# Optimization experiments

Measured on AMD Instinct MI355X. Metric: run time of the kernel, lower is better.

The kernel has to match this reference:

```python
import jax, jax.numpy as jnp
import numpy as np

B, E, H, W = 32, 512, 16, 16
NH, HD = 8, 64          # num_heads = embed_dim // num_heads_channels, head_dim = 64
OUT = 512
S = H * W + 1           # spacial_dim**2 + 1 = 257 (mean token prepended)


def setup_inputs() -> dict:
    key = jax.random.key(0)
    ks = jax.random.split(key, 10)
    sc = 1.0 / np.sqrt(E).astype(np.float32)
    n = lambda k, sh, s=1.0: jax.random.normal(k, sh, jnp.float32) * s
    return {
        "x_real": n(ks[0], (B, E, H, W)),
        "x_imag": n(ks[1], (B, E, H, W)),
        # positional_embedding = (randn/sqrt(E)).to(complex64) -> imag part is zero
        "pos_r": n(ks[2], (E, S), sc),
        "pos_i": jnp.zeros((E, S), jnp.float32),
        # complex in-projection (packed q,k,v) and out-projection of the MHA
        "w_in_r": n(ks[3], (3 * E, E), sc),
        "w_in_i": n(ks[4], (3 * E, E), sc),
        "b_in_r": jnp.zeros((3 * E,), jnp.float32),
        "b_in_i": jnp.zeros((3 * E,), jnp.float32),
        "w_out_r": n(ks[5], (E, E), sc),
        "w_out_i": n(ks[6], (E, E), sc),
        "b_out_r": jnp.zeros((E,), jnp.float32),
        "b_out_i": jnp.zeros((E,), jnp.float32),
        # complex 1x1 conv projection == complex linear over channels
        "w_p_r": n(ks[7], (OUT, E), sc),
        "w_p_i": n(ks[8], (OUT, E), sc),
        "b_p_r": jnp.zeros((OUT,), jnp.float32),
        "b_p_i": jnp.zeros((OUT,), jnp.float32),
    }


def _attention_pool(x_real, x_imag, pos_r, pos_i, w_in_r, w_in_i, b_in_r, b_in_i,
                    w_out_r, w_out_i, b_out_r, b_out_i, w_p_r, w_p_i, b_p_r, b_p_i):
    cx = jax.lax.complex
    x = cx(x_real, x_imag).reshape(B, E, -1)                       # [b,c,HW]
    x = jnp.concatenate([x.mean(-1, keepdims=True), x], axis=-1)   # [b,c,S]
    x = x + cx(pos_r, pos_i)[None]                                 # + pos embed
    x = x.transpose(0, 2, 1)                                       # [b,S,E]

    qkv = jnp.einsum('bse,fe->bsf', x, cx(w_in_r, w_in_i)) + cx(b_in_r, b_in_i)
    q, k, v = jnp.split(qkv, 3, axis=-1)
    q = q.reshape(B, S, NH, HD) / jnp.sqrt(jnp.float32(HD))
    k = k.reshape(B, S, NH, HD)
    v = v.reshape(B, S, NH, HD)

    logits = jnp.einsum('bqhd,bkhd->bhqk', q, k)                   # complex scores
    # complex softmax handled separately on real/imag parts
    w = cx(jax.nn.softmax(logits.real, axis=-1),
           jax.nn.softmax(logits.imag, axis=-1))
    attn = jnp.einsum('bhqk,bkhd->bqhd', w, v).reshape(B, S, E)
    attn = jnp.einsum('bse,fe->bsf', attn, cx(w_out_r, w_out_i)) + cx(b_out_r, b_out_i)

    y = attn.transpose(0, 2, 1)                                    # [b,E,S]
    y = jnp.einsum('oc,bcs->bos', cx(w_p_r, w_p_i), y) + cx(b_p_r, b_p_i)[None, :, None]
    return y[:, :, 0]                                              # [b,OUT] complex64


def reference(x_real, x_imag, pos_r, pos_i, w_in_r, w_in_i, b_in_r, b_in_i,
              w_out_r, w_out_i, b_out_r, b_out_i, w_p_r, w_p_i, b_p_r, b_p_i):
    return _attention_pool(x_real, x_imag, pos_r, pos_i, w_in_r, w_in_i, b_in_r,
                           b_in_i, w_out_r, w_out_i, b_out_r, b_out_i,
                           w_p_r, w_p_i, b_p_r, b_p_i)
```

## Files before the change

kernel.cpp:

```cpp
#include <hip/hip_runtime.h>

#define B_   32
#define E_   512
#define HW_  256
#define S_   257
#define NH_  8
#define HD_  64
#define ECH_ 16
#define NCH_ 32
#define NBLK 1024
#define NTHR 256
#define NGRP 32
#define GSZ  32

__device__ __forceinline__ void st_sys(float* p, float v) {
  __hip_atomic_store(p, v, __ATOMIC_RELAXED, __HIP_MEMORY_SCOPE_SYSTEM);
}
__device__ __forceinline__ void st_sys2(float2* p, float2 v) {
  unsigned long long u;
  __builtin_memcpy(&u, &v, 8);
  __hip_atomic_store((unsigned long long*)p, u, __ATOMIC_RELAXED, __HIP_MEMORY_SCOPE_SYSTEM);
}

__device__ __forceinline__ float wave_reduce(float v) {
  #pragma unroll
  for (int o = 32; o > 0; o >>= 1) v += __shfl_down(v, o, 64);
  return v;
}

__device__ __forceinline__ void gbar(unsigned* slots, int g, int j, int t, unsigned phase) {
  __syncthreads();
  if (t < 64) {
    if (t == 0)
      __hip_atomic_store(&slots[g * GSZ + j], phase, __ATOMIC_RELAXED, __HIP_MEMORY_SCOPE_SYSTEM);
    const unsigned* line = slots + g * GSZ;
    int sl = t & 31;
    for (;;) {
      unsigned v = __hip_atomic_load(&line[sl], __ATOMIC_RELAXED, __HIP_MEMORY_SCOPE_SYSTEM);
      if (__all((int)(v >= phase))) break;
      __builtin_amdgcn_s_sleep(2);
    }
  }
  __syncthreads();
}

__device__ void softmax257(float* l, float* red, int t) {
  float v = l[t];
  float v256 = l[256];
  red[t] = v; __syncthreads();
  #pragma unroll
  for (int s = 128; s > 0; s >>= 1) { if (t < s) red[t] = fmaxf(red[t], red[t + s]); __syncthreads(); }
  float M = fmaxf(red[0], v256);
  __syncthreads();
  float ex = expf(v - M);
  float e256 = expf(v256 - M);
  red[t] = ex; __syncthreads();
  #pragma unroll
  for (int s = 128; s > 0; s >>= 1) { if (t < s) red[t] += red[t + s]; __syncthreads(); }
  float inv = 1.f / (red[0] + e256);
  __syncthreads();
  l[t] = ex * inv;
  if (t == 0) l[256] = e256 * inv;
  __syncthreads();
}

__global__ __launch_bounds__(NTHR, 4) void k_mega(
    const float* __restrict__ xr, const float* __restrict__ xi,
    const float* __restrict__ pos_r, const float* __restrict__ pos_i,
    const float* __restrict__ w_in_r, const float* __restrict__ w_in_i,
    const float* __restrict__ b_in_r, const float* __restrict__ b_in_i,
    const float* __restrict__ w_out_r, const float* __restrict__ w_out_i,
    const float* __restrict__ b_out_r, const float* __restrict__ b_out_i,
    const float* __restrict__ w_p_r, const float* __restrict__ w_p_i,
    const float* __restrict__ b_p_r, const float* __restrict__ b_p_i,
    unsigned* slots,
    float* __restrict__ mr, float* __restrict__ mi,
    float* __restrict__ q0r, float* __restrict__ q0i,
    float* __restrict__ l0pr, float* __restrict__ l0pi,
    float* __restrict__ part, float* __restrict__ w2,
    float* __restrict__ zr_, float* __restrict__ zi_,
    float* __restrict__ a0r, float* __restrict__ a0i,
    float* __restrict__ aor, float* __restrict__ aoi,
    float* __restrict__ out, int interleaved) {
  __shared__ __align__(16) float smF[4112];
  const int t   = threadIdx.x;
  const int l   = t & 63;
  const int w   = t >> 6;
  const int bid = blockIdx.x;
  const int g   = bid >> 5;
  const int j   = bid & 31;

  #pragma unroll
  for (int rr = 0; rr < 4; ++rr) {
    int e = j * 16 + w * 4 + rr;
    float4 vr = ((const float4*)(xr + ((size_t)g * E_ + e) * HW_))[l];
    float4 vi = ((const float4*)(xi + ((size_t)g * E_ + e) * HW_))[l];
    float sr = (vr.x + vr.y) + (vr.z + vr.w);
    float si = (vi.x + vi.y) + (vi.z + vi.w);
    sr = wave_reduce(sr); si = wave_reduce(si);
    if (l == 0) {
      st_sys(&mr[g * E_ + e], sr * (1.f / HW_) + pos_r[(size_t)e * S_]);
      st_sys(&mi[g * E_ + e], si * (1.f / HW_) + pos_i[(size_t)e * S_]);
    }
  }
  gbar(slots, g, j, t, 1);

  {
    float* mR = smF;
    float* mI = smF + 512;
    mR[t]       = mr[g * E_ + t];        mI[t]       = mi[g * E_ + t];
    mR[t + 256] = mr[g * E_ + t + 256];  mI[t + 256] = mi[g * E_ + t + 256];
    __syncthreads();
    #pragma unroll
    for (int rr = 0; rr < 4; ++rr) {
      int f = j * 16 + w * 4 + rr;
      const float* wr = w_in_r + (size_t)f * E_;
      const float* wi = w_in_i + (size_t)f * E_;
      float ar = 0.f, ai = 0.f;
      #pragma unroll
      for (int e = l; e < E_; e += 64) {
        float Xr = mR[e], Xi = mI[e], Cr = wr[e], Ci = wi[e];
        ar += Xr * Cr - Xi * Ci;
        ai += Xr * Ci + Xi * Cr;
      }
      ar = wave_reduce(ar); ai = wave_reduce(ai);
      if (l == 0) {
        st_sys(&q0r[g * E_ + f], (ar + b_in_r[f]) * 0.125f);
        st_sys(&q0i[g * E_ + f], (ai + b_in_i[f]) * 0.125f);
      }
    }
  }
  gbar(slots, g, j, t, 2);

  {
    int c = j, e0 = c * ECH_;
    float* q0s = smF;
    float* us  = smF + 1024;
    float* mS  = smF + 1280;
    { int f0 = t * 2;
      q0s[f0 * 2 + 0]       = q0r[g * E_ + f0];
      q0s[f0 * 2 + 1]       = q0i[g * E_ + f0];
      q0s[(f0 + 1) * 2 + 0] = q0r[g * E_ + f0 + 1];
      q0s[(f0 + 1) * 2 + 1] = q0i[g * E_ + f0 + 1];
      if (t < ECH_) { mS[t * 2] = mr[g * E_ + e0 + t]; mS[t * 2 + 1] = mi[g * E_ + e0 + t]; }
    }
    __syncthreads();
    if (t < 128) {
      int e = t & 15, hh = t >> 4;
      float ar = 0.f, ai = 0.f;
      #pragma unroll 8
      for (int d = 0; d < HD_; ++d) {
        int f = hh * HD_ + d;
        float qr = q0s[f * 2], qi = q0s[f * 2 + 1];
        float Wr = w_in_r[(size_t)(E_ + f) * E_ + e0 + e];
        float Wi = w_in_i[(size_t)(E_ + f) * E_ + e0 + e];
        ar += qr * Wr - qi * Wi;
        ai += qr * Wi + qi * Wr;
      }
      us[(e * 8 + hh) * 2 + 0] = ar;
      us[(e * 8 + hh) * 2 + 1] = ai;
    }
    __syncthreads();
    if (t < NH_) {
      float pr = 0.f, pi = 0.f;
      #pragma unroll
      for (int e = 0; e < ECH_; ++e) {
        float Xr = mS[e * 2], Xi = mS[e * 2 + 1];
        float Ur = us[(e * 8 + t) * 2], Ui = us[(e * 8 + t) * 2 + 1];
        pr += Xr * Ur - Xi * Ui;
        pi += Xr * Ui + Xi * Ur;
      }
      st_sys(&l0pr[((size_t)g * NH_ + t) * NCH_ + c], pr);
      st_sys(&l0pi[((size_t)g * NH_ + t) * NCH_ + c], pi);
    }
    float ar[NH_], ai[NH_];
    #pragma unroll
    for (int hh = 0; hh < NH_; ++hh) { ar[hh] = 0.f; ai[hh] = 0.f; }
    const float* xrb = xr + ((size_t)g * E_ + e0) * HW_;
    const float* xib = xi + ((size_t)g * E_ + e0) * HW_;
    #pragma unroll 2
    for (int e = 0; e < ECH_; ++e) {
      float Xr = xrb[e * HW_ + t] + pos_r[(size_t)(e0 + e) * S_ + t + 1];
      float Xi = xib[e * HW_ + t] + pos_i[(size_t)(e0 + e) * S_ + t + 1];
      #pragma unroll
      for (int hh = 0; hh < NH_; ++hh) {
        float Ur = us[(e * 8 + hh) * 2], Ui = us[(e * 8 + hh) * 2 + 1];
        ar[hh] += Xr * Ur - Xi * Ui;
        ai[hh] += Xr * Ui + Xi * Ur;
      }
    }
    float2* p2 = (float2*)part;
    #pragma unroll
    for (int hh = 0; hh < NH_; ++hh) {
      float2 v; v.x = ar[hh]; v.y = ai[hh];
      st_sys2(&p2[(((size_t)g * NH_ + hh) * NCH_ + c) * 256 + t], v);
    }
  }
  gbar(slots, g, j, t, 3);

  if (j < NH_) {
    int bh = g * NH_ + j;
    float* lr  = smF;
    float* li  = smF + 260;
    float* red = smF + 520;
    const float2* p2 = (const float2*)part + (size_t)bh * NCH_ * 256;
    float sr = 0.f, si = 0.f;
    #pragma unroll
    for (int c = 0; c < NCH_; ++c) { float2 v = p2[c * 256 + t]; sr += v.x; si += v.y; }
    lr[t + 1] = sr; li[t + 1] = si;
    if (t < 64) {
      float v = (t < NCH_) ? l0pr[(size_t)bh * NCH_ + t] : 0.f;
      v = wave_reduce(v);
      if (t == 0) lr[0] = v;
    } else if (t < 128) {
      int tt = t - 64;
      float v = (tt < NCH_) ? l0pi[(size_t)bh * NCH_ + tt] : 0.f;
      v = wave_reduce(v);
      if (tt == 0) li[0] = v;
    }
    __syncthreads();
    softmax257(lr, red, t);
    softmax257(li, red, t);
    float2* o = (float2*)w2 + (size_t)bh * S_;
    float2 v; v.x = lr[t]; v.y = li[t];
    st_sys2(&o[t], v);
    if (t == 0) { float2 v2; v2.x = lr[256]; v2.y = li[256]; st_sys2(&o[256], v2); }
  }
  gbar(slots, g, j, t, 4);

  {
    float2* wls = (float2*)smF;
    const float2* w2b = (const float2*)w2 + (size_t)g * NH_ * S_;
    for (int i = t; i < NH_ * S_; i += NTHR) wls[i] = w2b[i];
    __syncthreads();
    #pragma unroll
    for (int sub = 0; sub < 2; ++sub) {
      int gq = j + sub * 32;
      #pragma unroll
      for (int r = 0; r < 2; ++r) {
        int e = gq * 8 + w * 2 + r;
        const float* xre = xr + ((size_t)g * E_ + e) * HW_;
        const float* xie = xi + ((size_t)g * E_ + e) * HW_;
        const float* pre = pos_r + (size_t)e * S_;
        const float* pie = pos_i + (size_t)e * S_;
        float ar2[NH_], ai2[NH_];
        #pragma unroll
        for (int hh = 0; hh < NH_; ++hh) { ar2[hh] = 0.f; ai2[hh] = 0.f; }
        #pragma unroll
        for (int jj = 0; jj < 4; ++jj) {
          int k = 1 + l + 64 * jj;
          float Xr = xre[k - 1] + pre[k];
          float Xi = xie[k - 1] + pie[k];
          #pragma unroll
          for (int hh = 0; hh < NH_; ++hh) {
            float2 W = wls[hh * S_ + k];
            ar2[hh] += W.x * Xr - W.y * Xi;
            ai2[hh] += W.x * Xi + W.y * Xr;
          }
        }
        #pragma unroll
        for (int hh = 0; hh < NH_; ++hh) { ar2[hh] = wave_reduce(ar2[hh]); ai2[hh] = wave_reduce(ai2[hh]); }
        if (l == 0) {
          float X0r = mr[g * E_ + e];
          float X0i = mi[g * E_ + e];
          #pragma unroll
          for (int hh = 0; hh < NH_; ++hh) {
            float2 W0 = wls[hh * S_];
            st_sys(&zr_[(size_t)(g * NH_ + hh) * E_ + e], ar2[hh] + W0.x * X0r - W0.y * X0i);
            st_sys(&zi_[(size_t)(g * NH_ + hh) * E_ + e], ai2[hh] + W0.x * X0i + W0.y * X0r);
          }
        }
      }
    }
  }
  gbar(slots, g, j, t, 5);

  #pragma unroll
  for (int rr = 0; rr < 4; ++rr) {
    int f = j * 16 + w * 4 + rr;
    int h = f >> 6;
    const float* wrp = w_in_r + (size_t)(2 * E_ + f) * E_;
    const float* wip = w_in_i + (size_t)(2 * E_ + f) * E_;
    const float* zrp = zr_ + (size_t)(g * NH_ + h) * E_;
    const float* zip = zi_ + (size_t)(g * NH_ + h) * E_;
    float ar = 0.f, ai = 0.f;
    #pragma unroll
    for (int e = l; e < E_; e += 64) {
      float Zr = zrp[e], Zi = zip[e], Cr = wrp[e], Ci = wip[e];
      ar += Zr * Cr - Zi * Ci;
      ai += Zr * Ci + Zi * Cr;
    }
    ar = wave_reduce(ar); ai = wave_reduce(ai);
    if (l == 0) {
      float bvr = b_in_r[2 * E_ + f], bvi = b_in_i[2 * E_ + f];
      st_sys(&a0r[g * E_ + f], ar + (bvr - bvi));
      st_sys(&a0i[g * E_ + f], ai + (bvr + bvi));
    }
  }
  gbar(slots, g, j, t, 6);

  #pragma unroll
  for (int rr = 0; rr < 4; ++rr) {
    int f = j * 16 + w * 4 + rr;
    const float* wrp = w_out_r + (size_t)f * E_;
    const float* wip = w_out_i + (size_t)f * E_;
    const float* ir = a0r + (size_t)g * E_;
    const float* ii = a0i + (size_t)g * E_;
    float ar = 0.f, ai = 0.f;
    #pragma unroll
    for (int e = l; e < E_; e += 64) {
      float Xr = ir[e], Xi = ii[e], Cr = wrp[e], Ci = wip[e];
      ar += Xr * Cr - Xi * Ci;
      ai += Xr * Ci + Xi * Cr;
    }
    ar = wave_reduce(ar); ai = wave_reduce(ai);
    if (l == 0) { st_sys(&aor[g * E_ + f], ar + b_out_r[f]); st_sys(&aoi[g * E_ + f], ai + b_out_i[f]); }
  }
  gbar(slots, g, j, t, 7);

  #pragma unroll
  for (int rr = 0; rr < 4; ++rr) {
    int f = j * 16 + w * 4 + rr;
    const float* wrp = w_p_r + (size_t)f * E_;
    const float* wip = w_p_i + (size_t)f * E_;
    const float* ir = aor + (size_t)g * E_;
    const float* ii = aoi + (size_t)g * E_;
    float ar = 0.f, ai = 0.f;
    #pragma unroll
    for (int e = l; e < E_; e += 64) {
      float Xr = ir[e], Xi = ii[e], Cr = wrp[e], Ci = wip[e];
      ar += Xr * Cr - Xi * Ci;
      ai += Xr * Ci + Xi * Cr;
    }
    ar = wave_reduce(ar); ai = wave_reduce(ai);
    if (l == 0) {
      float rr2 = ar + b_p_r[f];
      float im  = ai + b_p_i[f];
      int wid = g * E_ + f;
      if (interleaved) { out[(size_t)wid * 2] = rr2; out[(size_t)wid * 2 + 1] = im; }
      else             { out[wid] = rr2; }
    }
  }
}

extern "C" void kernel_launch(void* const* d_in, const int* in_sizes, int n_in,
                              void* d_out, int out_size, void* d_ws, size_t ws_size,
                              hipStream_t stream) {
  (void)in_sizes; (void)n_in; (void)ws_size;
  const float* xr      = (const float*)d_in[0];
  const float* xi      = (const float*)d_in[1];
  const float* pos_r   = (const float*)d_in[2];
  const float* pos_i   = (const float*)d_in[3];
  const float* w_in_r  = (const float*)d_in[4];
  const float* w_in_i  = (const float*)d_in[5];
  const float* b_in_r  = (const float*)d_in[6];
  const float* b_in_i  = (const float*)d_in[7];
  const float* w_out_r = (const float*)d_in[8];
  const float* w_out_i = (const float*)d_in[9];
  const float* b_out_r = (const float*)d_in[10];
  const float* b_out_i = (const float*)d_in[11];
  const float* w_p_r   = (const float*)d_in[12];
  const float* w_p_i   = (const float*)d_in[13];
  const float* b_p_r   = (const float*)d_in[14];
  const float* b_p_i   = (const float*)d_in[15];

  const int BE = B_ * E_, BHE = B_ * NH_ * E_;
  unsigned* slots = (unsigned*)d_ws;
  float* base = (float*)d_ws + 1024;
  float* mr   = base;
  float* mi   = mr   + BE;
  float* q0r  = mi   + BE;
  float* q0i  = q0r  + BE;
  float* l0pr = q0i  + BE;
  float* l0pi = l0pr + B_ * NH_ * NCH_;
  float* part = l0pi + B_ * NH_ * NCH_;
  float* w2   = part + (size_t)B_ * NH_ * NCH_ * 512;
  float* zr   = w2   + (size_t)2 * B_ * NH_ * S_;
  float* zi   = zr   + BHE;
  float* a0r  = zi   + BHE;
  float* a0i  = a0r  + BE;
  float* aor  = a0i  + BE;
  float* aoi  = aor  + BE;

  hipMemsetAsync(d_ws, 0, 4096, stream);
  k_mega<<<NBLK, NTHR, 0, stream>>>(
      xr, xi, pos_r, pos_i, w_in_r, w_in_i, b_in_r, b_in_i,
      w_out_r, w_out_i, b_out_r, b_out_i, w_p_r, w_p_i, b_p_r, b_p_i,
      slots, mr, mi, q0r, q0i, l0pr, l0pi, part, w2, zr, zi, a0r, a0i, aor, aoi,
      (float*)d_out, out_size >= 2 * B_ * E_);
}
```

Baseline: 202.3 us.

## Prefetch next-phase weights before barriers and use shuffle softmax reductions

```diff
diff --git a/kernel.cpp b/kernel.cpp
--- a/kernel.cpp
+++ b/kernel.cpp
@@ -45,20 +45,23 @@
 }
 
 __device__ void softmax257(float* l, float* red, int t) {
+  int lane = t & 63, wv = t >> 6;
   float v = l[t];
   float v256 = l[256];
-  red[t] = v; __syncthreads();
-  #pragma unroll
-  for (int s = 128; s > 0; s >>= 1) { if (t < s) red[t] = fmaxf(red[t], red[t + s]); __syncthreads(); }
-  float M = fmaxf(red[0], v256);
+  float m = v;
+  #pragma unroll
+  for (int o = 32; o > 0; o >>= 1) m = fmaxf(m, __shfl_xor(m, o, 64));
+  if (lane == 0) red[wv] = m;
   __syncthreads();
+  float M = fmaxf(fmaxf(fmaxf(red[0], red[1]), fmaxf(red[2], red[3])), v256);
   float ex = expf(v - M);
   float e256 = expf(v256 - M);
-  red[t] = ex; __syncthreads();
-  #pragma unroll
-  for (int s = 128; s > 0; s >>= 1) { if (t < s) red[t] += red[t + s]; __syncthreads(); }
-  float inv = 1.f / (red[0] + e256);
+  float s = ex;
+  #pragma unroll
+  for (int o = 32; o > 0; o >>= 1) s += __shfl_xor(s, o, 64);
+  if (lane == 0) red[4 + wv] = s;
   __syncthreads();
+  float inv = 1.f / (red[4] + red[5] + red[6] + red[7] + e256);
   l[t] = ex * inv;
   if (t == 0) l[256] = e256 * inv;
   __syncthreads();
@@ -89,6 +92,7 @@
   const int bid = blockIdx.x;
   const int g   = bid >> 5;
   const int j   = bid & 31;
+  float pfacc = 0.f;
 
   #pragma unroll
   for (int rr = 0; rr < 4; ++rr) {
@@ -103,6 +107,17 @@
       st_sys(&mi[g * E_ + e], si * (1.f / HW_) + pos_i[(size_t)e * S_]);
     }
   }
+  {
+    int row = 16 * j + (t >> 4);
+    int c32 = (t & 15) * 32;
+    pfacc += w_in_r[(size_t)row * E_ + c32] + w_in_i[(size_t)row * E_ + c32];
+    size_t colk = (size_t)16 * j;
+    pfacc += w_in_r[(size_t)(E_ + t) * E_ + colk] + w_in_i[(size_t)(E_ + t) * E_ + colk];
+    pfacc += w_in_r[(size_t)(E_ + t + 256) * E_ + colk] + w_in_i[(size_t)(E_ + t + 256) * E_ + colk];
+    int pcol = (t & 15) * 16 + 1;
+    pfacc += pos_r[(size_t)row * S_ + pcol] + pos_i[(size_t)row * S_ + pcol];
+  }
+  asm volatile("" :: "v"(pfacc));
   gbar(slots, g, j, t, 1);
 
   {
@@ -234,45 +249,45 @@
     for (int i = t; i < NH_ * S_; i += NTHR) wls[i] = w2b[i];
     __syncthreads();
     #pragma unroll
-    for (int sub = 0; sub < 2; ++sub) {
-      int gq = j + sub * 32;
-      #pragma unroll
-      for (int r = 0; r < 2; ++r) {
-        int e = gq * 8 + w * 2 + r;
-        const float* xre = xr + ((size_t)g * E_ + e) * HW_;
-        const float* xie = xi + ((size_t)g * E_ + e) * HW_;
-        const float* pre = pos_r + (size_t)e * S_;
-        const float* pie = pos_i + (size_t)e * S_;
-        float ar2[NH_], ai2[NH_];
+    for (int rr = 0; rr < 4; ++rr) {
+      int e = 16 * j + 4 * w + rr;
+      const float* xre = xr + ((size_t)g * E_ + e) * HW_;
+      const float* xie = xi + ((size_t)g * E_ + e) * HW_;
+      const float* pre = pos_r + (size_t)e * S_;
+      const float* pie = pos_i + (size_t)e * S_;
+      float ar2[NH_], ai2[NH_];
+      #pragma unroll
+      for (int hh = 0; hh < NH_; ++hh) { ar2[hh] = 0.f; ai2[hh] = 0.f; }
+      #pragma unroll
+      for (int jj = 0; jj < 4; ++jj) {
+        int k = 1 + l + 64 * jj;
+        float Xr = xre[k - 1] + pre[k];
+        float Xi = xie[k - 1] + pie[k];
         #pragma unroll
-        for (int hh = 0; hh < NH_; ++hh) { ar2[hh] = 0.f; ai2[hh] = 0.f; }
+        for (int hh = 0; hh < NH_; ++hh) {
+          float2 W = wls[hh * S_ + k];
+          ar2[hh] += W.x * Xr - W.y * Xi;
+          ai2[hh] += W.x * Xi + W.y * Xr;
+        }
+      }
+      #pragma unroll
+      for (int hh = 0; hh < NH_; ++hh) { ar2[hh] = wave_reduce(ar2[hh]); ai2[hh] = wave_reduce(ai2[hh]); }
+      if (l == 0) {
+        float X0r = mr[g * E_ + e];
+        float X0i = mi[g * E_ + e];
         #pragma unroll
-        for (int jj = 0; jj < 4; ++jj) {
-          int k = 1 + l + 64 * jj;
-          float Xr = xre[k - 1] + pre[k];
-          float Xi = xie[k - 1] + pie[k];
-          #pragma unroll
-          for (int hh = 0; hh < NH_; ++hh) {
-            float2 W = wls[hh * S_ + k];
-            ar2[hh] += W.x * Xr - W.y * Xi;
-            ai2[hh] += W.x * Xi + W.y * Xr;
-          }
+        for (int hh = 0; hh < NH_; ++hh) {
+          float2 W0 = wls[hh * S_];
+          st_sys(&zr_[(size_t)(g * NH_ + hh) * E_ + e], ar2[hh] + W0.x * X0r - W0.y * X0i);
+          st_sys(&zi_[(size_t)(g * NH_ + hh) * E_ + e], ai2[hh] + W0.x * X0i + W0.y * X0r);
         }
-        #pragma unroll
-        for (int hh = 0; hh < NH_; ++hh) { ar2[hh] = wave_reduce(ar2[hh]); ai2[hh] = wave_reduce(ai2[hh]); }
-        if (l == 0) {
-          float X0r = mr[g * E_ + e];
-          float X0i = mi[g * E_ + e];
-          #pragma unroll
-          for (int hh = 0; hh < NH_; ++hh) {
-            float2 W0 = wls[hh * S_];
-            st_sys(&zr_[(size_t)(g * NH_ + hh) * E_ + e], ar2[hh] + W0.x * X0r - W0.y * X0i);
-            st_sys(&zi_[(size_t)(g * NH_ + hh) * E_ + e], ai2[hh] + W0.x * X0i + W0.y * X0r);
-          }
-        }
-      }
-    }
-  }
+      }
+    }
+    int row = 16 * j + (t >> 4);
+    int c32 = (t & 15) * 32;
+    pfacc += w_in_r[(size_t)(2 * E_ + row) * E_ + c32] + w_in_i[(size_t)(2 * E_ + row) * E_ + c32];
+  }
+  asm volatile("" :: "v"(pfacc));
   gbar(slots, g, j, t, 5);
 
   #pragma unroll
@@ -297,6 +312,12 @@
       st_sys(&a0i[g * E_ + f], ai + (bvr + bvi));
     }
   }
+  {
+    int row = 16 * j + (t >> 4);
+    int c32 = (t & 15) * 32;
+    pfacc += w_out_r[(size_t)row * E_ + c32] + w_out_i[(size_t)row * E_ + c32];
+  }
+  asm volatile("" :: "v"(pfacc));
   gbar(slots, g, j, t, 6);
 
   #pragma unroll
@@ -316,6 +337,12 @@
     ar = wave_reduce(ar); ai = wave_reduce(ai);
     if (l == 0) { st_sys(&aor[g * E_ + f], ar + b_out_r[f]); st_sys(&aoi[g * E_ + f], ai + b_out_i[f]); }
   }
+  {
+    int row = 16 * j + (t >> 4);
+    int c32 = (t & 15) * 32;
+    pfacc += w_p_r[(size_t)row * E_ + c32] + w_p_i[(size_t)row * E_ + c32];
+  }
+  asm volatile("" :: "v"(pfacc));
   gbar(slots, g, j, t, 7);
 
   #pragma unroll
```

After: 212.9 us. 5.2% more time.

## Double block count per batch group and use wave-shuffle softmax reductions

Applied to the files above, without the earlier changes.

```diff
diff --git a/kernel.cpp b/kernel.cpp
--- a/kernel.cpp
+++ b/kernel.cpp
@@ -6,12 +6,12 @@
 #define S_   257
 #define NH_  8
 #define HD_  64
-#define ECH_ 16
-#define NCH_ 32
-#define NBLK 1024
+#define ECH_ 8
+#define NCH_ 64
+#define NBLK 2048
 #define NTHR 256
 #define NGRP 32
-#define GSZ  32
+#define GSZ  64
 
 __device__ __forceinline__ void st_sys(float* p, float v) {
   __hip_atomic_store(p, v, __ATOMIC_RELAXED, __HIP_MEMORY_SCOPE_SYSTEM);
@@ -34,9 +34,8 @@
     if (t == 0)
       __hip_atomic_store(&slots[g * GSZ + j], phase, __ATOMIC_RELAXED, __HIP_MEMORY_SCOPE_SYSTEM);
     const unsigned* line = slots + g * GSZ;
-    int sl = t & 31;
     for (;;) {
-      unsigned v = __hip_atomic_load(&line[sl], __ATOMIC_RELAXED, __HIP_MEMORY_SCOPE_SYSTEM);
+      unsigned v = __hip_atomic_load(&line[t], __ATOMIC_RELAXED, __HIP_MEMORY_SCOPE_SYSTEM);
       if (__all((int)(v >= phase))) break;
       __builtin_amdgcn_s_sleep(2);
     }
@@ -45,26 +44,29 @@
 }
 
 __device__ void softmax257(float* l, float* red, int t) {
+  int lane = t & 63, wv = t >> 6;
   float v = l[t];
   float v256 = l[256];
-  red[t] = v; __syncthreads();
-  #pragma unroll
-  for (int s = 128; s > 0; s >>= 1) { if (t < s) red[t] = fmaxf(red[t], red[t + s]); __syncthreads(); }
-  float M = fmaxf(red[0], v256);
-  __syncthreads();
+  float m = v;
+  #pragma unroll
+  for (int o = 32; o > 0; o >>= 1) m = fmaxf(m, __shfl_xor(m, o, 64));
+  if (lane == 0) red[wv] = m;
+  __syncthreads();
+  float M = fmaxf(fmaxf(fmaxf(red[0], red[1]), fmaxf(red[2], red[3])), v256);
   float ex = expf(v - M);
   float e256 = expf(v256 - M);
-  red[t] = ex; __syncthreads();
-  #pragma unroll
-  for (int s = 128; s > 0; s >>= 1) { if (t < s) red[t] += red[t + s]; __syncthreads(); }
-  float inv = 1.f / (red[0] + e256);
-  __syncthreads();
+  float s = ex;
+  #pragma unroll
+  for (int o = 32; o > 0; o >>= 1) s += __shfl_xor(s, o, 64);
+  if (lane == 0) red[4 + wv] = s;
+  __syncthreads();
+  float inv = 1.f / (red[4] + red[5] + red[6] + red[7] + e256);
   l[t] = ex * inv;
   if (t == 0) l[256] = e256 * inv;
   __syncthreads();
 }
 
-__global__ __launch_bounds__(NTHR, 4) void k_mega(
+__global__ __launch_bounds__(NTHR, 8) void k_mega(
     const float* __restrict__ xr, const float* __restrict__ xi,
     const float* __restrict__ pos_r, const float* __restrict__ pos_i,
     const float* __restrict__ w_in_r, const float* __restrict__ w_in_i,
@@ -87,12 +89,12 @@
   const int l   = t & 63;
   const int w   = t >> 6;
   const int bid = blockIdx.x;
-  const int g   = bid >> 5;
-  const int j   = bid & 31;
-
-  #pragma unroll
-  for (int rr = 0; rr < 4; ++rr) {
-    int e = j * 16 + w * 4 + rr;
+  const int g   = bid >> 6;
+  const int j   = bid & 63;
+
+  #pragma unroll
+  for (int rr = 0; rr < 2; ++rr) {
+    int e = j * 8 + w * 2 + rr;
     float4 vr = ((const float4*)(xr + ((size_t)g * E_ + e) * HW_))[l];
     float4 vi = ((const float4*)(xi + ((size_t)g * E_ + e) * HW_))[l];
     float sr = (vr.x + vr.y) + (vr.z + vr.w);
@@ -112,8 +114,8 @@
     mR[t + 256] = mr[g * E_ + t + 256];  mI[t + 256] = mi[g * E_ + t + 256];
     __syncthreads();
     #pragma unroll
-    for (int rr = 0; rr < 4; ++rr) {
-      int f = j * 16 + w * 4 + rr;
+    for (int rr = 0; rr < 2; ++rr) {
+      int f = j * 8 + w * 2 + rr;
       const float* wr = w_in_r + (size_t)f * E_;
       const float* wi = w_in_i + (size_t)f * E_;
       float ar = 0.f, ai = 0.f;
@@ -136,7 +138,8 @@
     int c = j, e0 = c * ECH_;
     float* q0s = smF;
     float* us  = smF + 1024;
-    float* mS  = smF + 1280;
+    float* pu  = smF + 1152;
+    float* mS  = smF + 1664;
     { int f0 = t * 2;
       q0s[f0 * 2 + 0]       = q0r[g * E_ + f0];
       q0s[f0 * 2 + 1]       = q0i[g * E_ + f0];
@@ -145,20 +148,27 @@
       if (t < ECH_) { mS[t * 2] = mr[g * E_ + e0 + t]; mS[t * 2 + 1] = mi[g * E_ + e0 + t]; }
     }
     __syncthreads();
-    if (t < 128) {
-      int e = t & 15, hh = t >> 4;
+    {
+      int e = t & 7, hh = (t >> 3) & 7, dq = t >> 6;
       float ar = 0.f, ai = 0.f;
-      #pragma unroll 8
-      for (int d = 0; d < HD_; ++d) {
-        int f = hh * HD_ + d;
+      #pragma unroll
+      for (int dd = 0; dd < 16; ++dd) {
+        int f = hh * HD_ + dq * 16 + dd;
         float qr = q0s[f * 2], qi = q0s[f * 2 + 1];
         float Wr = w_in_r[(size_t)(E_ + f) * E_ + e0 + e];
         float Wi = w_in_i[(size_t)(E_ + f) * E_ + e0 + e];
         ar += qr * Wr - qi * Wi;
         ai += qr * Wi + qi * Wr;
       }
-      us[(e * 8 + hh) * 2 + 0] = ar;
-      us[(e * 8 + hh) * 2 + 1] = ai;
+      pu[(dq * 64 + e * 8 + hh) * 2 + 0] = ar;
+      pu[(dq * 64 + e * 8 + hh) * 2 + 1] = ai;
+    }
+    __syncthreads();
+    if (t < 128) {
+      int e = t & 7, hh = (t >> 3) & 7, ri = t >> 6;
+      us[(e * 8 + hh) * 2 + ri] =
+          pu[(0 * 64 + e * 8 + hh) * 2 + ri] + pu[(1 * 64 + e * 8 + hh) * 2 + ri] +
+          pu[(2 * 64 + e * 8 + hh) * 2 + ri] + pu[(3 * 64 + e * 8 + hh) * 2 + ri];
     }
     __syncthreads();
     if (t < NH_) {
@@ -205,16 +215,16 @@
     float* red = smF + 520;
     const float2* p2 = (const float2*)part + (size_t)bh * NCH_ * 256;
     float sr = 0.f, si = 0.f;
-    #pragma unroll
+    #pragma unroll 8
     for (int c = 0; c < NCH_; ++c) { float2 v = p2[c * 256 + t]; sr += v.x; si += v.y; }
     lr[t + 1] = sr; li[t + 1] = si;
     if (t < 64) {
-      float v = (t < NCH_) ? l0pr[(size_t)bh * NCH_ + t] : 0.f;
+      float v = l0pr[(size_t)bh * NCH_ + t];
       v = wave_reduce(v);
       if (t == 0) lr[0] = v;
     } else if (t < 128) {
       int tt = t - 64;
-      float v = (tt < NCH_) ? l0pi[(size_t)bh * NCH_ + tt] : 0.f;
+      float v = l0pi[(size_t)bh * NCH_ + tt];
       v = wave_reduce(v);
       if (tt == 0) li[0] = v;
     }
@@ -234,50 +244,46 @@
     for (int i = t; i < NH_ * S_; i += NTHR) wls[i] = w2b[i];
     __syncthreads();
     #pragma unroll
-    for (int sub = 0; sub < 2; ++sub) {
-      int gq = j + sub * 32;
-      #pragma unroll
-      for (int r = 0; r < 2; ++r) {
-        int e = gq * 8 + w * 2 + r;
-        const float* xre = xr + ((size_t)g * E_ + e) * HW_;
-        const float* xie = xi + ((size_t)g * E_ + e) * HW_;
-        const float* pre = pos_r + (size_t)e * S_;
-        const float* pie = pos_i + (size_t)e * S_;
-        float ar2[NH_], ai2[NH_];
+    for (int rr = 0; rr < 2; ++rr) {
+      int e = 8 * j + 2 * w + rr;
+      const float* xre = xr + ((size_t)g * E_ + e) * HW_;
+      const float* xie = xi + ((size_t)g * E_ + e) * HW_;
+      const float* pre = pos_r + (size_t)e * S_;
+      const float* pie = pos_i + (size_t)e * S_;
+      float ar2[NH_], ai2[NH_];
+      #pragma unroll
+      for (int hh = 0; hh < NH_; ++hh) { ar2[hh] = 0.f; ai2[hh] = 0.f; }
+      #pragma unroll
+      for (int jj = 0; jj < 4; ++jj) {
+        int k = 1 + l + 64 * jj;
+        float Xr = xre[k - 1] + pre[k];
+        float Xi = xie[k - 1] + pie[k];
         #pragma unroll
-        for (int hh = 0; hh < NH_; ++hh) { ar2[hh] = 0.f; ai2[hh] = 0.f; }
+        for (int hh = 0; hh < NH_; ++hh) {
+          float2 W = wls[hh * S_ + k];
+          ar2[hh] += W.x * Xr - W.y * Xi;
+          ai2[hh] += W.x * Xi + W.y * Xr;
+        }
+      }
+      #pragma unroll
+      for (int hh = 0; hh < NH_; ++hh) { ar2[hh] = wave_reduce(ar2[hh]); ai2[hh] = wave_reduce(ai2[hh]); }
+      if (l == 0) {
+        float X0r = mr[g * E_ + e];
+        float X0i = mi[g * E_ + e];
         #pragma unroll
-        for (int jj = 0; jj < 4; ++jj) {
-          int k = 1 + l + 64 * jj;
-          float Xr = xre[k - 1] + pre[k];
-          float Xi = xie[k - 1] + pie[k];
-          #pragma unroll
-          for (int hh = 0; hh < NH_; ++hh) {
-            float2 W = wls[hh * S_ + k];
-            ar2[hh] += W.x * Xr - W.y * Xi;
-            ai2[hh] += W.x * Xi + W.y * Xr;
-          }
+        for (int hh = 0; hh < NH_; ++hh) {
+          float2 W0 = wls[hh * S_];
+          st_sys(&zr_[(size_t)(g * NH_ + hh) * E_ + e], ar2[hh] + W0.x * X0r - W0.y * X0i);
+          st_sys(&zi_[(size_t)(g * NH_ + hh) * E_ + e], ai2[hh] + W0.x * X0i + W0.y * X0r);
         }
-        #pragma unroll
-        for (int hh = 0; hh < NH_; ++hh) { ar2[hh] = wave_reduce(ar2[hh]); ai2[hh] = wave_reduce(ai2[hh]); }
-        if (l == 0) {
-          float X0r = mr[g * E_ + e];
-          float X0i = mi[g * E_ + e];
-          #pragma unroll
-          for (int hh = 0; hh < NH_; ++hh) {
-            float2 W0 = wls[hh * S_];
-            st_sys(&zr_[(size_t)(g * NH_ + hh) * E_ + e], ar2[hh] + W0.x * X0r - W0.y * X0i);
-            st_sys(&zi_[(size_t)(g * NH_ + hh) * E_ + e], ai2[hh] + W0.x * X0i + W0.y * X0r);
-          }
-        }
       }
     }
   }
   gbar(slots, g, j, t, 5);
 
   #pragma unroll
-  for (int rr = 0; rr < 4; ++rr) {
-    int f = j * 16 + w * 4 + rr;
+  for (int rr = 0; rr < 2; ++rr) {
+    int f = j * 8 + w * 2 + rr;
     int h = f >> 6;
     const float* wrp = w_in_r + (size_t)(2 * E_ + f) * E_;
     const float* wip = w_in_i + (size_t)(2 * E_ + f) * E_;
@@ -300,8 +306,8 @@
   gbar(slots, g, j, t, 6);
 
   #pragma unroll
-  for (int rr = 0; rr < 4; ++rr) {
-    int f = j * 16 + w * 4 + rr;
+  for (int rr = 0; rr < 2; ++rr) {
+    int f = j * 8 + w * 2 + rr;
     const float* wrp = w_out_r + (size_t)f * E_;
     const float* wip = w_out_i + (size_t)f * E_;
     const float* ir = a0r + (size_t)g * E_;
@@ -319,8 +325,8 @@
   gbar(slots, g, j, t, 7);
 
   #pragma unroll
-  for (int rr = 0; rr < 4; ++rr) {
-    int f = j * 16 + w * 4 + rr;
+  for (int rr = 0; rr < 2; ++rr) {
+    int f = j * 8 + w * 2 + rr;
     const float* wrp = w_p_r + (size_t)f * E_;
     const float* wip = w_p_i + (size_t)f * E_;
     const float* ir = aor + (size_t)g * E_;
@@ -366,7 +372,7 @@
 
   const int BE = B_ * E_, BHE = B_ * NH_ * E_;
   unsigned* slots = (unsigned*)d_ws;
-  float* base = (float*)d_ws + 1024;
+  float* base = (float*)d_ws + 4096;
   float* mr   = base;
   float* mi   = mr   + BE;
   float* q0r  = mi   + BE;
@@ -382,7 +388,7 @@
   float* aor  = a0i  + BE;
   float* aoi  = aor  + BE;
 
-  hipMemsetAsync(d_ws, 0, 4096, stream);
+  hipMemsetAsync(d_ws, 0, 16384, stream);
   k_mega<<<NBLK, NTHR, 0, stream>>>(
       xr, xi, pos_r, pos_i, w_in_r, w_in_i, b_in_r, b_in_i,
       w_out_r, w_out_i, b_out_r, b_out_i, w_p_r, w_p_i, b_p_r, b_p_i,
```

Result: slower. 284.4 us (+40.6%).

## Fuse q0 and key-weight product via atomics, drop partial-logit buffers, shuffle softmax

Applied to the files above, without the earlier changes.

```diff
diff --git a/kernel.cpp b/kernel.cpp
--- a/kernel.cpp
+++ b/kernel.cpp
@@ -5,13 +5,11 @@
 #define HW_  256
 #define S_   257
 #define NH_  8
-#define HD_  64
-#define ECH_ 16
-#define NCH_ 32
 #define NBLK 1024
 #define NTHR 256
 #define NGRP 32
 #define GSZ  32
+#define LG_  260
 
 __device__ __forceinline__ void st_sys(float* p, float v) {
   __hip_atomic_store(p, v, __ATOMIC_RELAXED, __HIP_MEMORY_SCOPE_SYSTEM);
@@ -45,20 +43,23 @@
 }
 
 __device__ void softmax257(float* l, float* red, int t) {
+  int lane = t & 63, wv = t >> 6;
   float v = l[t];
   float v256 = l[256];
-  red[t] = v; __syncthreads();
-  #pragma unroll
-  for (int s = 128; s > 0; s >>= 1) { if (t < s) red[t] = fmaxf(red[t], red[t + s]); __syncthreads(); }
-  float M = fmaxf(red[0], v256);
-  __syncthreads();
+  float m = v;
+  #pragma unroll
+  for (int o = 32; o > 0; o >>= 1) m = fmaxf(m, __shfl_xor(m, o, 64));
+  if (lane == 0) red[wv] = m;
+  __syncthreads();
+  float M = fmaxf(fmaxf(fmaxf(red[0], red[1]), fmaxf(red[2], red[3])), v256);
   float ex = expf(v - M);
   float e256 = expf(v256 - M);
-  red[t] = ex; __syncthreads();
-  #pragma unroll
-  for (int s = 128; s > 0; s >>= 1) { if (t < s) red[t] += red[t + s]; __syncthreads(); }
-  float inv = 1.f / (red[0] + e256);
-  __syncthreads();
+  float s = ex;
+  #pragma unroll
+  for (int o = 32; o > 0; o >>= 1) s += __shfl_xor(s, o, 64);
+  if (lane == 0) red[4 + wv] = s;
+  __syncthreads();
+  float inv = 1.f / (red[4] + red[5] + red[6] + red[7] + e256);
   l[t] = ex * inv;
   if (t == 0) l[256] = e256 * inv;
   __syncthreads();
@@ -74,10 +75,10 @@
     const float* __restrict__ w_p_r, const float* __restrict__ w_p_i,
     const float* __restrict__ b_p_r, const float* __restrict__ b_p_i,
     unsigned* slots,
+    float* __restrict__ ur_, float* __restrict__ ui_,
+    float* __restrict__ lgr, float* __restrict__ lgi,
     float* __restrict__ mr, float* __restrict__ mi,
-    float* __restrict__ q0r, float* __restrict__ q0i,
-    float* __restrict__ l0pr, float* __restrict__ l0pi,
-    float* __restrict__ part, float* __restrict__ w2,
+    float* __restrict__ w2,
     float* __restrict__ zr_, float* __restrict__ zi_,
     float* __restrict__ a0r, float* __restrict__ a0i,
     float* __restrict__ aor, float* __restrict__ aoi,
@@ -106,14 +107,16 @@
   gbar(slots, g, j, t, 1);
 
   {
-    float* mR = smF;
-    float* mI = smF + 512;
+    float* mR  = smF;
+    float* mI  = smF + 512;
+    float* q0L = smF + 1024;
     mR[t]       = mr[g * E_ + t];        mI[t]       = mi[g * E_ + t];
     mR[t + 256] = mr[g * E_ + t + 256];  mI[t + 256] = mi[g * E_ + t + 256];
     __syncthreads();
     #pragma unroll
     for (int rr = 0; rr < 4; ++rr) {
-      int f = j * 16 + w * 4 + rr;
+      int fl = w * 4 + rr;
+      int f  = 16 * j + fl;
       const float* wr = w_in_r + (size_t)f * E_;
       const float* wi = w_in_i + (size_t)f * E_;
       float ar = 0.f, ai = 0.f;
@@ -125,61 +128,45 @@
       }
       ar = wave_reduce(ar); ai = wave_reduce(ai);
       if (l == 0) {
-        st_sys(&q0r[g * E_ + f], (ar + b_in_r[f]) * 0.125f);
-        st_sys(&q0i[g * E_ + f], (ai + b_in_i[f]) * 0.125f);
-      }
-    }
+        q0L[fl * 2]     = (ar + b_in_r[f]) * 0.125f;
+        q0L[fl * 2 + 1] = (ai + b_in_i[f]) * 0.125f;
+      }
+    }
+    __syncthreads();
+    int h = j >> 2;
+    float u0r = 0.f, u0i = 0.f, u1r = 0.f, u1i = 0.f;
+    #pragma unroll 4
+    for (int fl = 0; fl < 16; ++fl) {
+      int f = 16 * j + fl;
+      float qr = q0L[fl * 2], qi = q0L[fl * 2 + 1];
+      const float* Wr = w_in_r + (size_t)(E_ + f) * E_;
+      const float* Wi = w_in_i + (size_t)(E_ + f) * E_;
+      float W0r = Wr[t], W0i = Wi[t], W1r = Wr[t + 256], W1i = Wi[t + 256];
+      u0r += qr * W0r - qi * W0i;  u0i += qr * W0i + qi * W0r;
+      u1r += qr * W1r - qi * W1i;  u1i += qr * W1i + qi * W1r;
+    }
+    size_t ub = (size_t)(g * NH_ + h) * E_;
+    atomicAdd(&ur_[ub + t], u0r);        atomicAdd(&ui_[ub + t], u0i);
+    atomicAdd(&ur_[ub + t + 256], u1r);  atomicAdd(&ui_[ub + t + 256], u1i);
   }
   gbar(slots, g, j, t, 2);
 
   {
-    int c = j, e0 = c * ECH_;
-    float* q0s = smF;
-    float* us  = smF + 1024;
-    float* mS  = smF + 1280;
-    { int f0 = t * 2;
-      q0s[f0 * 2 + 0]       = q0r[g * E_ + f0];
-      q0s[f0 * 2 + 1]       = q0i[g * E_ + f0];
-      q0s[(f0 + 1) * 2 + 0] = q0r[g * E_ + f0 + 1];
-      q0s[(f0 + 1) * 2 + 1] = q0i[g * E_ + f0 + 1];
-      if (t < ECH_) { mS[t * 2] = mr[g * E_ + e0 + t]; mS[t * 2 + 1] = mi[g * E_ + e0 + t]; }
-    }
-    __syncthreads();
+    int e0 = 16 * j;
+    float* us = smF;
     if (t < 128) {
       int e = t & 15, hh = t >> 4;
-      float ar = 0.f, ai = 0.f;
-      #pragma unroll 8
-      for (int d = 0; d < HD_; ++d) {
-        int f = hh * HD_ + d;
-        float qr = q0s[f * 2], qi = q0s[f * 2 + 1];
-        float Wr = w_in_r[(size_t)(E_ + f) * E_ + e0 + e];
-        float Wi = w_in_i[(size_t)(E_ + f) * E_ + e0 + e];
-        ar += qr * Wr - qi * Wi;
-        ai += qr * Wi + qi * Wr;
-      }
-      us[(e * 8 + hh) * 2 + 0] = ar;
-      us[(e * 8 + hh) * 2 + 1] = ai;
-    }
-    __syncthreads();
-    if (t < NH_) {
-      float pr = 0.f, pi = 0.f;
-      #pragma unroll
-      for (int e = 0; e < ECH_; ++e) {
-        float Xr = mS[e * 2], Xi = mS[e * 2 + 1];
-        float Ur = us[(e * 8 + t) * 2], Ui = us[(e * 8 + t) * 2 + 1];
-        pr += Xr * Ur - Xi * Ui;
-        pi += Xr * Ui + Xi * Ur;
-      }
-      st_sys(&l0pr[((size_t)g * NH_ + t) * NCH_ + c], pr);
-      st_sys(&l0pi[((size_t)g * NH_ + t) * NCH_ + c], pi);
-    }
+      us[(e * 8 + hh) * 2]     = ur_[(size_t)(g * NH_ + hh) * E_ + e0 + e];
+      us[(e * 8 + hh) * 2 + 1] = ui_[(size_t)(g * NH_ + hh) * E_ + e0 + e];
+    }
+    __syncthreads();
     float ar[NH_], ai[NH_];
     #pragma unroll
     for (int hh = 0; hh < NH_; ++hh) { ar[hh] = 0.f; ai[hh] = 0.f; }
     const float* xrb = xr + ((size_t)g * E_ + e0) * HW_;
     const float* xib = xi + ((size_t)g * E_ + e0) * HW_;
     #pragma unroll 2
-    for (int e = 0; e < ECH_; ++e) {
+    for (int e = 0; e < 16; ++e) {
       float Xr = xrb[e * HW_ + t] + pos_r[(size_t)(e0 + e) * S_ + t + 1];
       float Xi = xib[e * HW_ + t] + pos_i[(size_t)(e0 + e) * S_ + t + 1];
       #pragma unroll
@@ -189,11 +176,11 @@
         ai[hh] += Xr * Ui + Xi * Ur;
       }
     }
-    float2* p2 = (float2*)part;
     #pragma unroll
     for (int hh = 0; hh < NH_; ++hh) {
-      float2 v; v.x = ar[hh]; v.y = ai[hh];
-      st_sys2(&p2[(((size_t)g * NH_ + hh) * NCH_ + c) * 256 + t], v);
+      size_t lb = (size_t)(g * NH_ + hh) * LG_ + t + 1;
+      atomicAdd(&lgr[lb], ar[hh]);
+      atomicAdd(&lgi[lb], ai[hh]);
     }
   }
   gbar(slots, g, j, t, 3);
@@ -202,29 +189,38 @@
     int bh = g * NH_ + j;
     float* lr  = smF;
     float* li  = smF + 260;
-    float* red = smF + 520;
-    const float2* p2 = (const float2*)part + (size_t)bh * NCH_ * 256;
-    float sr = 0.f, si = 0.f;
-    #pragma unroll
-    for (int c = 0; c < NCH_; ++c) { float2 v = p2[c * 256 + t]; sr += v.x; si += v.y; }
-    lr[t + 1] = sr; li[t + 1] = si;
-    if (t < 64) {
-      float v = (t < NCH_) ? l0pr[(size_t)bh * NCH_ + t] : 0.f;
-      v = wave_reduce(v);
-      if (t == 0) lr[0] = v;
-    } else if (t < 128) {
-      int tt = t - 64;
-      float v = (tt < NCH_) ? l0pi[(size_t)bh * NCH_ + tt] : 0.f;
-      v = wave_reduce(v);
-      if (tt == 0) li[0] = v;
-    }
-    __syncthreads();
-    softmax257(lr, red, t);
-    softmax257(li, red, t);
+    float* redl = smF + 520;
+    float* reds = smF + 528;
+    lr[t + 1] = lgr[(size_t)bh * LG_ + t + 1];
+    li[t + 1] = lgi[(size_t)bh * LG_ + t + 1];
+    float pr = 0.f, pi = 0.f;
+    #pragma unroll
+    for (int e = t; e < E_; e += 256) {
+      float Xr = mr[g * E_ + e], Xi = mi[g * E_ + e];
+      float Ur = ur_[(size_t)bh * E_ + e], Ui = ui_[(size_t)bh * E_ + e];
+      pr += Xr * Ur - Xi * Ui;
+      pi += Xr * Ui + Xi * Ur;
+    }
+    pr = wave_reduce(pr); pi = wave_reduce(pi);
+    if (l == 0) { redl[w * 2] = pr; redl[w * 2 + 1] = pi; }
+    __syncthreads();
+    if (t == 0) {
+      lr[0] = redl[0] + redl[2] + redl[4] + redl[6];
+      li[0] = redl[1] + redl[3] + redl[5] + redl[7];
+    }
+    __syncthreads();
+    softmax257(lr, reds, t);
+    softmax257(li, reds, t);
     float2* o = (float2*)w2 + (size_t)bh * S_;
     float2 v; v.x = lr[t]; v.y = li[t];
     st_sys2(&o[t], v);
     if (t == 0) { float2 v2; v2.x = lr[256]; v2.y = li[256]; st_sys2(&o[256], v2); }
+  } else {
+    int idx = t & 127;
+    int e = 16 * j + (idx & 15);
+    const float* src = (t < 128) ? xr : xi;
+    float pf = src[((size_t)g * E_ + e) * HW_ + (idx >> 4) * 32];
+    asm volatile("" :: "v"(pf));
   }
   gbar(slots, g, j, t, 4);
 
@@ -234,41 +230,37 @@
     for (int i = t; i < NH_ * S_; i += NTHR) wls[i] = w2b[i];
     __syncthreads();
     #pragma unroll
-    for (int sub = 0; sub < 2; ++sub) {
-      int gq = j + sub * 32;
-      #pragma unroll
-      for (int r = 0; r < 2; ++r) {
-        int e = gq * 8 + w * 2 + r;
-        const float* xre = xr + ((size_t)g * E_ + e) * HW_;
-        const float* xie = xi + ((size_t)g * E_ + e) * HW_;
-        const float* pre = pos_r + (size_t)e * S_;
-        const float* pie = pos_i + (size_t)e * S_;
-        float ar2[NH_], ai2[NH_];
+    for (int rr = 0; rr < 4; ++rr) {
+      int e = 16 * j + 4 * w + rr;
+      const float* xre = xr + ((size_t)g * E_ + e) * HW_;
+      const float* xie = xi + ((size_t)g * E_ + e) * HW_;
+      const float* pre = pos_r + (size_t)e * S_;
+      const float* pie = pos_i + (size_t)e * S_;
+      float ar2[NH_], ai2[NH_];
+      #pragma unroll
+      for (int hh = 0; hh < NH_; ++hh) { ar2[hh] = 0.f; ai2[hh] = 0.f; }
+      #pragma unroll
+      for (int jj = 0; jj < 4; ++jj) {
+        int k = 1 + l + 64 * jj;
+        float Xr = xre[k - 1] + pre[k];
+        float Xi = xie[k - 1] + pie[k];
         #pragma unroll
-        for (int hh = 0; hh < NH_; ++hh) { ar2[hh] = 0.f; ai2[hh] = 0.f; }
+        for (int hh = 0; hh < NH_; ++hh) {
+          float2 W = wls[hh * S_ + k];
+          ar2[hh] += W.x * Xr - W.y * Xi;
+          ai2[hh] += W.x * Xi + W.y * Xr;
+        }
+      }
+      #pragma unroll
+      for (int hh = 0; hh < NH_; ++hh) { ar2[hh] = wave_reduce(ar2[hh]); ai2[hh] = wave_reduce(ai2[hh]); }
+      if (l == 0) {
+        float X0r = mr[g * E_ + e];
+        float X0i = mi[g * E_ + e];
         #pragma unroll
-        for (int jj = 0; jj < 4; ++jj) {
-          int k = 1 + l + 64 * jj;
-          float Xr = xre[k - 1] + pre[k];
-          float Xi = xie[k - 1] + pie[k];
-          #pragma unroll
-          for (int hh = 0; hh < NH_; ++hh) {
-            float2 W = wls[hh * S_ + k];
-            ar2[hh] += W.x * Xr - W.y * Xi;
-            ai2[hh] += W.x * Xi + W.y * Xr;
-          }
-        }
-        #pragma unroll
-        for (int hh = 0; hh < NH_; ++hh) { ar2[hh] = wave_reduce(ar2[hh]); ai2[hh] = wave_reduce(ai2[hh]); }
-        if (l == 0) {
-          float X0r = mr[g * E_ + e];
-          float X0i = mi[g * E_ + e];
-          #pragma unroll
-          for (int hh = 0; hh < NH_; ++hh) {
-            float2 W0 = wls[hh * S_];
-            st_sys(&zr_[(size_t)(g * NH_ + hh) * E_ + e], ar2[hh] + W0.x * X0r - W0.y * X0i);
-            st_sys(&zi_[(size_t)(g * NH_ + hh) * E_ + e], ai2[hh] + W0.x * X0i + W0.y * X0r);
-          }
+        for (int hh = 0; hh < NH_; ++hh) {
+          float2 W0 = wls[hh * S_];
+          st_sys(&zr_[(size_t)(g * NH_ + hh) * E_ + e], ar2[hh] + W0.x * X0r - W0.y * X0i);
+          st_sys(&zi_[(size_t)(g * NH_ + hh) * E_ + e], ai2[hh] + W0.x * X0i + W0.y * X0r);
         }
       }
     }
@@ -365,27 +357,27 @@
   const float* b_p_i   = (const float*)d_in[15];
 
   const int BE = B_ * E_, BHE = B_ * NH_ * E_;
+  float* ws = (float*)d_ws;
   unsigned* slots = (unsigned*)d_ws;
-  float* base = (float*)d_ws + 1024;
-  float* mr   = base;
-  float* mi   = mr   + BE;
-  float* q0r  = mi   + BE;
-  float* q0i  = q0r  + BE;
-  float* l0pr = q0i  + BE;
-  float* l0pi = l0pr + B_ * NH_ * NCH_;
-  float* part = l0pi + B_ * NH_ * NCH_;
-  float* w2   = part + (size_t)B_ * NH_ * NCH_ * 512;
-  float* zr   = w2   + (size_t)2 * B_ * NH_ * S_;
-  float* zi   = zr   + BHE;
-  float* a0r  = zi   + BHE;
-  float* a0i  = a0r  + BE;
-  float* aor  = a0i  + BE;
-  float* aoi  = aor  + BE;
-
-  hipMemsetAsync(d_ws, 0, 4096, stream);
+  float* ur   = ws + 1024;
+  float* ui   = ur + BHE;
+  float* lgr  = ui + BHE;
+  float* lgi  = lgr + B_ * NH_ * LG_;
+  float* mr   = lgi + B_ * NH_ * LG_;
+  float* mi   = mr + BE;
+  float* w2   = mi + BE;
+  float* zr   = w2 + (size_t)2 * B_ * NH_ * S_;
+  float* zi   = zr + BHE;
+  float* a0r  = zi + BHE;
+  float* a0i  = a0r + BE;
+  float* aor  = a0i + BE;
+  float* aoi  = aor + BE;
+
+  size_t zbytes = (size_t)(1024 + 2 * BHE + 2 * B_ * NH_ * LG_) * 4;
+  hipMemsetAsync(d_ws, 0, zbytes, stream);
   k_mega<<<NBLK, NTHR, 0, stream>>>(
       xr, xi, pos_r, pos_i, w_in_r, w_in_i, b_in_r, b_in_i,
       w_out_r, w_out_i, b_out_r, b_out_i, w_p_r, w_p_i, b_p_r, b_p_i,
-      slots, mr, mi, q0r, q0i, l0pr, l0pi, part, w2, zr, zi, a0r, a0i, aor, aoi,
+      slots, ur, ui, lgr, lgi, mr, mi, w2, zr, zi, a0r, a0i, aor, aoi,
       (float*)d_out, out_size >= 2 * B_ * E_);
 }
```

New measurement: 204.6 us. About the same (+1.1%).
